# Optimization experiments

Hardware: AMD Instinct MI355X
Metric: run time of the kernel (lower is better)

Reference implementation:

```python
import jax, jax.numpy as jnp
import numpy as np

B, SD, SE, DM, H, DK, DV, DFF = 4, 2048, 2048, 1024, 8, 128, 128, 4096
NEG = -jnp.inf


def _linear(x, w, b):
    # torch nn.Linear: w [out, in]
    return jnp.einsum('...i,oi->...o', x, w) + b


def _layer_norm(x, g, b, eps=1e-5):
    mu = jnp.mean(x, axis=-1, keepdims=True)
    var = jnp.var(x, axis=-1, keepdims=True)
    return (x - mu) * jax.lax.rsqrt(var + eps) * g + b


def _mha(Q, K, V, wq, bq, wk, bk, wv, bv, wo, bo, pad_mask, seq_mask):
    # wq/wk: [H, DK, DM], wv: [H, DV, DM]; vectorized over the per-head Linears
    Qh = jnp.einsum('bsd,hkd->bhsk', Q, wq) + bq[None, :, None, :]  # [B,H,Sq,DK]
    Kh = jnp.einsum('bsd,hkd->bhsk', K, wk) + bk[None, :, None, :]  # [B,H,Sk,DK]
    Vh = jnp.einsum('bsd,hvd->bhsv', V, wv) + bv[None, :, None, :]  # [B,H,Sk,DV]
    scores = jnp.einsum('bhqd,bhkd->bhqk', Qh, Kh) / np.sqrt(DK)
    scores = jnp.where(pad_mask[:, None, :, :] == 0, NEG, scores)
    if seq_mask is not None:
        scores = jnp.where(seq_mask[None, None, :, :] == 0, NEG, scores)
    w = jax.nn.softmax(scores, axis=-1)
    out = jnp.einsum('bhqk,bhkv->bhqv', w, Vh)  # [B,H,Sq,DV]
    out = out.transpose(0, 2, 1, 3).reshape(Q.shape[0], Q.shape[1], H * DV)
    return _linear(out, wo, bo)


def setup_inputs() -> dict:
    key = jax.random.key(0)
    ks = iter(jax.random.split(key, 40))
    s = 0.02
    d = {
        'output_embs': jax.random.normal(next(ks), (B, SD, DM), jnp.float32),
        'encoder_output': jax.random.normal(next(ks), (B, SE, DM), jnp.float32),
        'inputs_padding_mask': jnp.ones((B, 1, SE), jnp.int32),
        'outputs_padding_mask': jnp.ones((B, 1, SD), jnp.int32),
    }
    for name in ['q1', 'k1', 'v1', 'q2', 'k2', 'v2']:
        d[name + '_w'] = jax.random.normal(next(ks), (DM, DM), jnp.float32) * s
        d[name + '_b'] = jnp.zeros((DM,), jnp.float32)
    for p in ['sa', 'ed']:
        d[p + '_qw'] = jax.random.normal(next(ks), (H, DK, DM), jnp.float32) * s
        d[p + '_qb'] = jnp.zeros((H, DK), jnp.float32)
        d[p + '_kw'] = jax.random.normal(next(ks), (H, DK, DM), jnp.float32) * s
        d[p + '_kb'] = jnp.zeros((H, DK), jnp.float32)
        d[p + '_vw'] = jax.random.normal(next(ks), (H, DV, DM), jnp.float32) * s
        d[p + '_vb'] = jnp.zeros((H, DV), jnp.float32)
        d[p + '_ow'] = jax.random.normal(next(ks), (DM, H * DV), jnp.float32) * s
        d[p + '_ob'] = jnp.zeros((DM,), jnp.float32)
    d['ff_w1'] = jax.random.normal(next(ks), (DFF, DM), jnp.float32) * s
    d['ff_b1'] = jnp.zeros((DFF,), jnp.float32)
    d['ff_w2'] = jax.random.normal(next(ks), (DM, DFF), jnp.float32) * s
    d['ff_b2'] = jnp.zeros((DM,), jnp.float32)
    d['ln1_g'] = jnp.ones((DM,), jnp.float32)
    d['ln1_b'] = jnp.zeros((DM,), jnp.float32)
    d['ln2_g'] = jnp.ones((DM,), jnp.float32)
    d['ln2_b'] = jnp.zeros((DM,), jnp.float32)
    return d


def reference(output_embs, encoder_output, inputs_padding_mask, outputs_padding_mask,
              q1_w, q1_b, k1_w, k1_b, v1_w, v1_b,
              q2_w, q2_b, k2_w, k2_b, v2_w, v2_b,
              sa_qw, sa_qb, sa_kw, sa_kb, sa_vw, sa_vb, sa_ow, sa_ob,
              ed_qw, ed_qb, ed_kw, ed_kb, ed_vw, ed_vb, ed_ow, ed_ob,
              ff_w1, ff_b1, ff_w2, ff_b2, ln1_g, ln1_b, ln2_g, ln2_b):
    # Dropout (p=0.1 in torch) treated as identity for a deterministic reference.
    seq_len = output_embs.shape[1]
    seq_mask = jnp.tril(jnp.ones((seq_len, seq_len), jnp.float32))
    Q = _linear(output_embs, q1_w, q1_b)
    K = _linear(output_embs, k1_w, k1_b)
    V = _linear(output_embs, v1_w, v1_b)
    x = output_embs + _mha(Q, K, V, sa_qw, sa_qb, sa_kw, sa_kb, sa_vw, sa_vb,
                           sa_ow, sa_ob, outputs_padding_mask, seq_mask)
    x = _layer_norm(x, ln1_g, ln1_b)
    Q2 = _linear(x, q2_w, q2_b)
    K2 = _linear(encoder_output, k2_w, k2_b)
    V2 = _linear(encoder_output, v2_w, v2_b)
    # NOTE: original adds residual from output_embs (not x) -- kept faithful.
    y = output_embs + _mha(Q2, K2, V2, ed_qw, ed_qb, ed_kw, ed_kb, ed_vw, ed_vb,
                           ed_ow, ed_ob, inputs_padding_mask, None)
    y = _layer_norm(y, ln2_g, ln2_b)
    ff = _linear(jax.nn.relu(_linear(y, ff_w1, ff_b1)), ff_w2, ff_b2)
    out = y + ff
    # original reuses layer_norm2 for the final norm (layer_norm3 unused) -- faithful.
    out = _layer_norm(out, ln2_g, ln2_b)
    return out
```

## Files before the change

kernel.cpp:

```cpp
#include <hip/hip_runtime.h>
#include <hip/hip_bf16.h>

typedef __hip_bfloat16 bf16;
typedef short short8 __attribute__((ext_vector_type(8)));
typedef short short4v __attribute__((ext_vector_type(4)));
typedef float floatx4 __attribute__((ext_vector_type(4)));
typedef int intx4 __attribute__((ext_vector_type(4)));
typedef unsigned int uintx4 __attribute__((ext_vector_type(4)));

#define B_ 4
#define SD_ 2048
#define SE_ 2048
#define DM_ 1024
#define H_ 8
#define DFF_ 4096

__device__ __forceinline__ float b2f(bf16 v) { return __bfloat162float(v); }
__device__ __forceinline__ bf16 f2b(float v) { return __float2bfloat16(v); }
__device__ __forceinline__ short f2s(float v) { return __builtin_bit_cast(short, __float2bfloat16(v)); }

__device__ __forceinline__ unsigned cvtpk_bf16(float lo, float hi) {
    unsigned r;
    asm("v_cvt_pk_bf16_f32 %0, %1, %2" : "=v"(r) : "v"(lo), "v"(hi));
    return r;
}
__device__ __forceinline__ void pl32swap(unsigned &x, unsigned &y) {
    asm("v_permlane32_swap_b32 %0, %1" : "+v"(x), "+v"(y));
}
__device__ __forceinline__ void pl16swap(unsigned &x, unsigned &y) {
    asm("v_permlane16_swap_b32 %0, %1" : "+v"(x), "+v"(y));
}

__device__ __forceinline__ void gl_lds16(const short* g, short* l) {
    __builtin_amdgcn_global_load_lds(
        (const __attribute__((address_space(1))) void*)g,
        (__attribute__((address_space(3))) void*)l, 16, 0, 0);
}

__global__ __launch_bounds__(256) void cvt_f32_bf16(
    const float* __restrict__ in, bf16* __restrict__ out, int n)
{
    int i = (blockIdx.x * 256 + threadIdx.x) * 8;
    if (i >= n) return;
    floatx4 a = *(const floatx4*)(in + i);
    floatx4 b = *(const floatx4*)(in + i + 4);
    short8 r;
#pragma unroll
    for (int k = 0; k < 4; ++k) { r[k] = f2s(a[k]); r[k + 4] = f2s(b[k]); }
    *(short8*)(out + i) = r;
}

__global__ __launch_bounds__(256) void cvt_f32_bf16_T(
    const float* __restrict__ in, bf16* __restrict__ out)
{
    __shared__ short tl[32][36];
    const int tid = threadIdx.x;
    const int i = tid >> 3;
    const int j = (tid & 7) * 4;
    const int r0 = blockIdx.x * 32, c0 = blockIdx.y * 32;
    floatx4 v = *(const floatx4*)(in + (size_t)(r0 + i) * 1024 + c0 + j);
#pragma unroll
    for (int p = 0; p < 4; ++p) tl[i][j + p] = f2s(v[p]);
    __syncthreads();
    short4v r;
#pragma unroll
    for (int p = 0; p < 4; ++p) r[p] = tl[j + p][i];
    *(short4v*)(out + (size_t)(c0 + i) * 1024 + r0 + j) = r;
}

__global__ __launch_bounds__(256) void bias_comp(
    const float* __restrict__ w, const float* __restrict__ bin,
    const float* __restrict__ badd, float* __restrict__ out)
{
    __shared__ float red[4];
    const int o = blockIdx.x;
    const int t = threadIdx.x;
    float s = 0.f;
#pragma unroll
    for (int i = t; i < 1024; i += 256) s += w[(size_t)o * 1024 + i] * bin[i];
#pragma unroll
    for (int off = 32; off >= 1; off >>= 1) s += __shfl_xor(s, off);
    if ((t & 63) == 0) red[t >> 6] = s;
    __syncthreads();
    if (t == 0) out[o] = red[0] + red[1] + red[2] + red[3] + badd[o];
}

template <int RELU>
__global__ __launch_bounds__(256) void gemm_bt(
    const bf16* __restrict__ A, const bf16* __restrict__ W,
    const float* __restrict__ bias, bf16* __restrict__ C,
    int M, int N, int K)
{
    __shared__ __align__(16) short As[16 * 512];
    __shared__ __align__(16) short Ws[16 * 512];

    const int tid  = threadIdx.x;
    const int lane = tid & 63;
    const int wave = tid >> 6;
    const int quad = lane >> 4;
    const int l16  = lane & 15;
    const int r7   = l16 & 7;
    const int bm0  = blockIdx.y * 128;
    const int bn0  = blockIdx.x * 128;
    const int wm   = (wave >> 1) * 64;
    const int wn   = (wave & 1) * 64;

    const int scol = (((lane & 7) ^ (lane >> 3)) * 8);
    const short* Ag = (const short*)A + (size_t)(bm0 + wave * 32 + (lane >> 3)) * K + scol;
    const short* Wg = (const short*)W + (size_t)(bn0 + wave * 32 + (lane >> 3)) * K + scol;
    short* Al = As + (wave * 4) * 512;
    short* Wl = Ws + (wave * 4) * 512;

    floatx4 acc[4][4];
#pragma unroll
    for (int i = 0; i < 4; ++i)
#pragma unroll
        for (int j = 0; j < 4; ++j)
            acc[i][j] = (floatx4){0.f, 0.f, 0.f, 0.f};

    for (int k0 = 0; k0 < K; k0 += 64) {
        __syncthreads();
#pragma unroll
        for (int s = 0; s < 4; ++s) {
            gl_lds16(Ag + k0 + (size_t)s * 8 * K, Al + s * 512);
            gl_lds16(Wg + k0 + (size_t)s * 8 * K, Wl + s * 512);
        }
        __syncthreads();
#pragma unroll
        for (int kk = 0; kk < 64; kk += 32) {
            short8 af[4], bg[4];
#pragma unroll
            for (int i = 0; i < 4; ++i) {
                int row = wm + i * 16 + l16;
                af[i] = *(const short8*)&As[(row >> 3) * 512 + r7 * 64 +
                                            (((quad + (kk >> 3)) ^ r7) << 3)];
            }
#pragma unroll
            for (int j = 0; j < 4; ++j) {
                int row = wn + j * 16 + l16;
                bg[j] = *(const short8*)&Ws[(row >> 3) * 512 + r7 * 64 +
                                            (((quad + (kk >> 3)) ^ r7) << 3)];
            }
#pragma unroll
            for (int i = 0; i < 4; ++i)
#pragma unroll
                for (int j = 0; j < 4; ++j)
                    acc[i][j] = __builtin_amdgcn_mfma_f32_16x16x32_bf16(
                        af[i], bg[j], acc[i][j], 0, 0, 0);
        }
    }

#pragma unroll
    for (int j = 0; j < 4; ++j) {
        int col = bn0 + wn + j * 16 + l16;
        float bv = bias ? bias[col] : 0.f;
#pragma unroll
        for (int i = 0; i < 4; ++i) {
            int row0 = bm0 + wm + i * 16 + quad * 4;
#pragma unroll
            for (int r = 0; r < 4; ++r) {
                float v = acc[i][j][r] + bv;
                if (RELU) v = fmaxf(v, 0.f);
                C[(size_t)(row0 + r) * N + col] = f2b(v);
            }
        }
    }
}

template <int RELU>
__global__ __launch_bounds__(512, 2) void gemm256(
    const bf16* __restrict__ A, const bf16* __restrict__ W,
    const float* __restrict__ bias, bf16* __restrict__ C,
    int M, int N, int K)
{
    __shared__ __align__(16) short L[3 * 24576];

    const int tid  = threadIdx.x;
    const int lane = tid & 63;
    const int wave = tid >> 6;
    const int quad = lane >> 4;
    const int l16  = lane & 15;
    const int r7   = l16 & 7;
    const int wm   = wave >> 1;
    const int wn   = wave & 1;

    const int gx  = gridDim.x;
    const int nwg = gx * gridDim.y;
    int wg = blockIdx.y * gx + blockIdx.x;
    if ((nwg & 7) == 0) wg = (wg & 7) * (nwg >> 3) + (wg >> 3);
    const int bn0 = (wg % gx) * 128;
    const int bm0 = (wg / gx) * 256;

    const int scol = (((lane & 7) ^ ((lane >> 3) & 7)) * 8);
    const short* Ag = (const short*)A + (size_t)(bm0 + wave * 32 + (lane >> 3)) * K + scol;
    const short* Wg = (const short*)W + (size_t)(bn0 + wave * 16 + (lane >> 3)) * K + scol;
    const int aw = (wave * 32) * 64;
    const int bw = 16384 + (wave * 16) * 64;

    floatx4 acc[4][4];
#pragma unroll
    for (int i = 0; i < 4; ++i)
#pragma unroll
        for (int j = 0; j < 4; ++j)
            acc[i][j] = (floatx4){0.f, 0.f, 0.f, 0.f};

    const int T = K / 64;

#pragma unroll
    for (int i = 0; i < 4; ++i) gl_lds16(Ag + (size_t)(i * 8) * K, L + aw + i * 8 * 64);
#pragma unroll
    for (int i = 0; i < 2; ++i) gl_lds16(Wg + (size_t)(i * 8) * K, L + bw + i * 8 * 64);
#pragma unroll
    for (int i = 0; i < 4; ++i) gl_lds16(Ag + 64 + (size_t)(i * 8) * K, L + 24576 + aw + i * 8 * 64);
#pragma unroll
    for (int i = 0; i < 2; ++i) gl_lds16(Wg + 64 + (size_t)(i * 8) * K, L + 24576 + bw + i * 8 * 64);
    asm volatile("s_waitcnt vmcnt(6)" ::: "memory");
    __builtin_amdgcn_s_barrier();

    int cur = 0, stg = 2;
    for (int t = 0; t < T; ++t) {
        __builtin_amdgcn_sched_barrier(0);
        const int kt = (t + 2 < T) ? (t + 2) : (T - 1);
        const size_t kg = (size_t)kt * 64;
        const short* Ac = L + cur * 24576;
        const short* Bc = Ac + 16384;
        short* As_s = L + stg * 24576 + aw;
        short* Bs_s = L + stg * 24576 + bw;

        short8 af[2][2], bf[4][2];

#pragma unroll
        for (int mi = 0; mi < 2; ++mi)
#pragma unroll
            for (int ks = 0; ks < 2; ++ks)
                af[mi][ks] = *(const short8*)&Ac[(wm * 64 + mi * 16 + l16) * 64 +
                                                (((ks * 4 + quad) ^ r7) << 3)];
#pragma unroll
        for (int nf = 0; nf < 4; ++nf)
#pragma unroll
            for (int ks = 0; ks < 2; ++ks)
                bf[nf][ks] = *(const short8*)&Bc[(wn * 64 + nf * 16 + l16) * 64 +
                                                (((ks * 4 + quad) ^ r7) << 3)];
        gl_lds16(Ag + kg, As_s);
        gl_lds16(Ag + kg + (size_t)8 * K, As_s + 8 * 64);
        gl_lds16(Wg + kg, Bs_s);
        __builtin_amdgcn_s_barrier();
        asm volatile("s_waitcnt lgkmcnt(0)" ::: "memory");
        __builtin_amdgcn_sched_barrier(0);
        __builtin_amdgcn_s_setprio(1);
#pragma unroll
        for (int ks = 0; ks < 2; ++ks)
#pragma unroll
            for (int mi = 0; mi < 2; ++mi)
#pragma unroll
                for (int nf = 0; nf < 4; ++nf)
                    acc[mi][nf] = __builtin_amdgcn_mfma_f32_16x16x32_bf16(
                        af[mi][ks], bf[nf][ks], acc[mi][nf], 0, 0, 0);
        __builtin_amdgcn_s_setprio(0);
        __builtin_amdgcn_s_barrier();

#pragma unroll
        for (int mi = 0; mi < 2; ++mi)
#pragma unroll
            for (int ks = 0; ks < 2; ++ks)
                af[mi][ks] = *(const short8*)&Ac[(wm * 64 + (2 + mi) * 16 + l16) * 64 +
                                                (((ks * 4 + quad) ^ r7) << 3)];
        gl_lds16(Ag + kg + (size_t)16 * K, As_s + 16 * 64);
        gl_lds16(Ag + kg + (size_t)24 * K, As_s + 24 * 64);
        gl_lds16(Wg + kg + (size_t)8 * K, Bs_s + 8 * 64);
        __builtin_amdgcn_s_barrier();
        asm volatile("s_waitcnt lgkmcnt(0)" ::: "memory");
        __builtin_amdgcn_sched_barrier(0);
        __builtin_amdgcn_s_setprio(1);
#pragma unroll
        for (int ks = 0; ks < 2; ++ks)
#pragma unroll
            for (int mi = 0; mi < 2; ++mi)
#pragma unroll
                for (int nf = 0; nf < 4; ++nf)
                    acc[2 + mi][nf] = __builtin_amdgcn_mfma_f32_16x16x32_bf16(
                        af[mi][ks], bf[nf][ks], acc[2 + mi][nf], 0, 0, 0);
        __builtin_amdgcn_s_setprio(0);
        asm volatile("s_waitcnt vmcnt(6)" ::: "memory");
        __builtin_amdgcn_s_barrier();

        cur = (cur == 2) ? 0 : cur + 1;
        stg = (stg == 2) ? 0 : stg + 1;
    }

#pragma unroll
    for (int nf = 0; nf < 4; ++nf) {
        int col = bn0 + wn * 64 + nf * 16 + l16;
        float bv = bias ? bias[col] : 0.f;
#pragma unroll
        for (int mf = 0; mf < 4; ++mf) {
            int row0 = bm0 + wm * 64 + mf * 16 + quad * 4;
#pragma unroll
            for (int r = 0; r < 4; ++r) {
                float v = acc[mf][nf][r] + bv;
                if (RELU) v = fmaxf(v, 0.f);
                C[(size_t)(row0 + r) * N + col] = f2b(v);
            }
        }
    }
}

__global__ __launch_bounds__(256) void vtrans(
    const bf16* __restrict__ in, int str, bf16* __restrict__ out, int S)
{
    __shared__ short t[32][36];
    const int tid = threadIdx.x;
    const int s0  = blockIdx.x * 32;
    const int d0  = blockIdx.y * 32;
    const int bh  = blockIdx.z;
    const int b = bh >> 3, h = bh & 7;
    const int i = tid >> 3;
    const int j = (tid & 7) * 4;

    *(short4v*)&t[i][j] =
        *(const short4v*)(in + (size_t)(b * S + s0 + i) * str + h * 128 + d0 + j);
    __syncthreads();
    short4v r;
#pragma unroll
    for (int p = 0; p < 4; ++p) r[p] = t[j + p][i];
    *(short4v*)(out + ((size_t)bh * 128 + d0 + i) * S + s0 + j) = r;
}

template <int CAUSAL>
__global__ __launch_bounds__(256) void flash_attn(
    const bf16* __restrict__ Q, int qstr, const bf16* __restrict__ K, int kstr,
    const bf16* __restrict__ Vt, const int* __restrict__ pad,
    bf16* __restrict__ Of, float* __restrict__ Ls, int Sq, int Sk)
{
    __shared__ __align__(16) short Ks[64 * 128];
    __shared__ __align__(16) short Vs[128 * 64];

    const int tid  = threadIdx.x;
    const int lane = tid & 63;
    const int wave = tid >> 6;
    const int quad = lane >> 4;
    const int l16  = lane & 15;
    const int r7   = l16 & 7;
    const int bh   = blockIdx.y;
    const int b    = bh >> 3;
    const int h    = bh & 7;
    const int par  = blockIdx.z;
    int tile = blockIdx.x;
    if (CAUSAL) tile = (tile & 1) ? (gridDim.x - 1 - (tile >> 1)) : (tile >> 1);
    const int q0 = tile * 128;
    const int qw = q0 + wave * 32;

    short8 qf[2][4];
#pragma unroll
    for (int mi = 0; mi < 2; ++mi) {
        const bf16* qb = Q + (size_t)(b * Sq + qw + mi * 16 + l16) * qstr + h * 128;
#pragma unroll
        for (int c = 0; c < 4; ++c)
            qf[mi][c] = *(const short8*)(qb + c * 32 + quad * 8);
    }

    floatx4 o[2][8];
#pragma unroll
    for (int mi = 0; mi < 2; ++mi)
#pragma unroll
        for (int nf = 0; nf < 8; ++nf) o[mi][nf] = (floatx4){0.f, 0.f, 0.f, 0.f};
    float lsum[2] = {0.f, 0.f};

    const float sc = 0.08838834764831845f * 1.4426950408889634f;
    int kEnd = Sk;
    if (CAUSAL && q0 + 128 < Sk) kEnd = q0 + 128;

    const bf16* vb0 = Vt + (size_t)bh * 128 * Sk;

    for (int ci = par; ci * 64 < kEnd; ci += 2) {
        const int kc = ci * 64;
        __syncthreads();
#pragma unroll
        for (int s = 0; s < 4; ++s) {
            int seg = wave * 4 + s;
            int kr = seg * 4 + (lane >> 4);
            int kg = (lane & 15) ^ (kr & 7);
            gl_lds16((const short*)K + (size_t)(b * Sk + kc + kr) * kstr + h * 128 + kg * 8,
                     Ks + seg * 512);
            int vr = seg * 8 + (lane >> 3);
            int vg = (lane & 7) ^ (vr & 7);
            gl_lds16((const short*)vb0 + (size_t)vr * Sk + kc + vg * 8,
                     Vs + seg * 512);
        }
        __syncthreads();

        short8 pfm[2][2];
#pragma unroll
        for (int c = 0; c < 2; ++c) {
            floatx4 sT[2][2];
#pragma unroll
            for (int fp = 0; fp < 2; ++fp) {
                const int f = c * 2 + fp;
                const int krow = f * 16 + l16;
                short8 kf[4];
#pragma unroll
                for (int cc = 0; cc < 4; ++cc)
                    kf[cc] = *(const short8*)&Ks[krow * 128 + (((cc * 4 + quad) ^ r7) << 3)];
#pragma unroll
                for (int mi = 0; mi < 2; ++mi) {
                    floatx4 s = (floatx4){0.f, 0.f, 0.f, 0.f};
#pragma unroll
                    for (int cc = 0; cc < 4; ++cc)
                        s = __builtin_amdgcn_mfma_f32_16x16x32_bf16(
                            kf[cc], qf[mi][cc], s, 0, 0, 0);
                    sT[mi][fp] = s;
                }
            }

            const int* pb = pad + (size_t)b * Sk + kc + c * 32 + quad * 4;
            intx4 pv0 = *(const intx4*)pb;
            intx4 pv1 = *(const intx4*)(pb + 16);

#pragma unroll
            for (int mi = 0; mi < 2; ++mi) {
                const int qv = qw + mi * 16 + l16;
#pragma unroll
                for (int fp = 0; fp < 2; ++fp) {
#pragma unroll
                    for (int r = 0; r < 4; ++r) {
                        int kk = kc + (c * 2 + fp) * 16 + quad * 4 + r;
                        bool ok = ((fp ? pv1[r] : pv0[r]) != 0);
                        if (CAUSAL) ok = ok && (kk <= qv);
                        float p = ok ? __builtin_amdgcn_exp2f(sT[mi][fp][r] * sc) : 0.f;
                        sT[mi][fp][r] = p;
                        lsum[mi] += p;
                    }
                }
                unsigned wA = cvtpk_bf16(sT[mi][0][0], sT[mi][0][1]);
                unsigned wB = cvtpk_bf16(sT[mi][0][2], sT[mi][0][3]);
                unsigned wC = cvtpk_bf16(sT[mi][1][0], sT[mi][1][1]);
                unsigned wD = cvtpk_bf16(sT[mi][1][2], sT[mi][1][3]);
                pl32swap(wA, wC);
                pl16swap(wA, wC);
                pl32swap(wB, wD);
                pl16swap(wB, wD);
                uintx4 t;
                t[0] = wA; t[1] = wB; t[2] = wC; t[3] = wD;
                pfm[mi][c] = __builtin_bit_cast(short8, t);
            }
        }

#pragma unroll
        for (int nf = 0; nf < 8; ++nf) {
            int vrow = nf * 16 + l16;
            short8 vf0 = *(const short8*)&Vs[vrow * 64 + ((quad ^ r7) << 3)];
            short8 vf1 = *(const short8*)&Vs[vrow * 64 + (((4 + quad) ^ r7) << 3)];
#pragma unroll
            for (int mi = 0; mi < 2; ++mi) {
                o[mi][nf] = __builtin_amdgcn_mfma_f32_16x16x32_bf16(
                    pfm[mi][0], vf0, o[mi][nf], 0, 0, 0);
                o[mi][nf] = __builtin_amdgcn_mfma_f32_16x16x32_bf16(
                    pfm[mi][1], vf1, o[mi][nf], 0, 0, 0);
            }
        }
    }

    bf16* op = Of + (size_t)par * B_ * Sq * DM_;
    float* lp = Ls + (size_t)par * B_ * H_ * Sq;
#pragma unroll
    for (int mi = 0; mi < 2; ++mi) {
        float s = lsum[mi];
        s += __shfl_xor(s, 16);
        s += __shfl_xor(s, 32);
        if (lane < 16)
            lp[(size_t)bh * Sq + qw + mi * 16 + l16] = s;
#pragma unroll
        for (int nf = 0; nf < 8; ++nf)
#pragma unroll
            for (int r = 0; r < 4; ++r) {
                int q = qw + mi * 16 + quad * 4 + r;
                op[(size_t)(b * Sq + q) * DM_ + h * 128 + nf * 16 + l16] =
                    f2b(o[mi][nf][r]);
            }
    }
}

__global__ __launch_bounds__(256) void attn_combine(
    const bf16* __restrict__ Of, const float* __restrict__ Ls,
    bf16* __restrict__ out)
{
    const int row = blockIdx.x;
    const int t = threadIdx.x;
    const int col = t * 4;
    const int h = col >> 7;
    const int b = row >> 11;
    const int q = row & (SD_ - 1);
    const size_t NV = (size_t)B_ * SD_ * DM_;
    const int idx = (b * H_ + h) * SD_ + q;
    float l = Ls[idx] + Ls[B_ * H_ * SD_ + idx];
    float inv = l > 0.f ? 1.f / l : 0.f;
    size_t base = (size_t)row * DM_ + col;
    short4v a0 = *(const short4v*)(Of + base);
    short4v a1 = *(const short4v*)(Of + NV + base);
    short4v r;
#pragma unroll
    for (int i = 0; i < 4; ++i)
        r[i] = f2s((b2f(__builtin_bit_cast(bf16, (short)a0[i])) +
                    b2f(__builtin_bit_cast(bf16, (short)a1[i]))) * inv);
    *(short4v*)(out + base) = r;
}

template <int A32, int O32>
__global__ __launch_bounds__(256) void add_ln(
    const void* __restrict__ Ap, const bf16* __restrict__ Bv,
    const float* __restrict__ g, const float* __restrict__ be,
    void* __restrict__ outp)
{
    const int D = DM_;
    __shared__ float red[8];
    const size_t row = blockIdx.x;
    const int t = threadIdx.x;

    float x[4];
    {
        float av[4];
        if (A32) {
            floatx4 a4 = *(const floatx4*)((const float*)Ap + row * D + t * 4);
#pragma unroll
            for (int i = 0; i < 4; ++i) av[i] = a4[i];
        } else {
            short4v a4 = *(const short4v*)((const bf16*)Ap + row * D + t * 4);
#pragma unroll
            for (int i = 0; i < 4; ++i)
                av[i] = b2f(__builtin_bit_cast(bf16, (short)a4[i]));
        }
        short4v b4 = *(const short4v*)(Bv + row * D + t * 4);
#pragma unroll
        for (int i = 0; i < 4; ++i)
            x[i] = av[i] + b2f(__builtin_bit_cast(bf16, (short)b4[i]));
    }
    float s = 0.f, s2 = 0.f;
#pragma unroll
    for (int i = 0; i < 4; ++i) { s += x[i]; s2 += x[i] * x[i]; }
#pragma unroll
    for (int off = 32; off >= 1; off >>= 1) {
        s  += __shfl_xor(s, off);
        s2 += __shfl_xor(s2, off);
    }
    const int wave = t >> 6;
    if ((t & 63) == 0) { red[wave] = s; red[4 + wave] = s2; }
    __syncthreads();
    s  = red[0] + red[1] + red[2] + red[3];
    s2 = red[4] + red[5] + red[6] + red[7];
    const float mu   = s * (1.f / D);
    const float var  = s2 * (1.f / D) - mu * mu;
    const float rstd = rsqrtf(var + 1e-5f);
#pragma unroll
    for (int i = 0; i < 4; ++i) {
        int idx = t * 4 + i;
        float v = (x[i] - mu) * rstd * g[idx] + be[idx];
        if (O32) ((float*)outp)[row * D + idx] = v;
        else     ((bf16*)outp)[row * D + idx] = f2b(v);
    }
}

extern "C" void kernel_launch(void* const* d_in, const int* in_sizes, int n_in,
                              void* d_out, int out_size, void* d_ws, size_t ws_size,
                              hipStream_t stream)
{
    const float* emb    = (const float*)d_in[0];
    const float* enc    = (const float*)d_in[1];
    const int*  in_pad  = (const int*)d_in[2];
    const int*  out_pad = (const int*)d_in[3];
    const float* q1_w = (const float*)d_in[4];  const float* q1_b = (const float*)d_in[5];
    const float* k1_w = (const float*)d_in[6];  const float* k1_b = (const float*)d_in[7];
    const float* v1_w = (const float*)d_in[8];  const float* v1_b = (const float*)d_in[9];
    const float* q2_w = (const float*)d_in[10]; const float* q2_b = (const float*)d_in[11];
    const float* k2_w = (const float*)d_in[12]; const float* k2_b = (const float*)d_in[13];
    const float* v2_w = (const float*)d_in[14]; const float* v2_b = (const float*)d_in[15];
    const float* sa_qw = (const float*)d_in[16]; const float* sa_qb = (const float*)d_in[17];
    const float* sa_kw = (const float*)d_in[18]; const float* sa_kb = (const float*)d_in[19];
    const float* sa_vw = (const float*)d_in[20]; const float* sa_vb = (const float*)d_in[21];
    const float* sa_ow = (const float*)d_in[22]; const float* sa_ob = (const float*)d_in[23];
    const float* ed_qw = (const float*)d_in[24]; const float* ed_qb = (const float*)d_in[25];
    const float* ed_kw = (const float*)d_in[26]; const float* ed_kb = (const float*)d_in[27];
    const float* ed_vw = (const float*)d_in[28]; const float* ed_vb = (const float*)d_in[29];
    const float* ed_ow = (const float*)d_in[30]; const float* ed_ob = (const float*)d_in[31];
    const float* ff_w1 = (const float*)d_in[32]; const float* ff_b1 = (const float*)d_in[33];
    const float* ff_w2 = (const float*)d_in[34]; const float* ff_b2 = (const float*)d_in[35];
    const float* ln1_g = (const float*)d_in[36]; const float* ln1_b = (const float*)d_in[37];
    const float* ln2_g = (const float*)d_in[38]; const float* ln2_b = (const float*)d_in[39];

    const int M = B_ * SD_;
    const size_t MM = (size_t)1024 * 1024;
    bf16* ws = (bf16*)d_ws;

    bf16* Wqkv = ws;
    bf16* Wkv  = ws + 3 * MM;
    bf16* Wq2  = ws + 5 * MM;
    bf16* Wso  = ws + 6 * MM;
    bf16* Weo  = ws + 7 * MM;
    bf16* Wf1  = ws + 8 * MM;
    bf16* Wf2  = ws + 12 * MM;
    float* bQKV = (float*)(ws + 16 * MM);
    float* bKV  = bQKV + 3072;
    float* bQ2  = bKV + 2048;
    float* Lsum = bQ2 + 2048;
    bf16* hw   = ws + 17 * MM;
    bf16* ft   = ws + 23 * MM;
    bf16* emb_b = ws + 17 * MM;
    bf16* enc_b = ws + 25 * MM;
    bf16* sqkv  = ws + 33 * MM;
    bf16* skv   = ws + 33 * MM;
    bf16* sq2   = ws + 49 * MM;
    bf16* sVt   = ws + 57 * MM;
    bf16* attn  = ws + 65 * MM;
    bf16* Ofb   = ws + 73 * MM;
    bf16* s1    = ws + 73 * MM;
    bf16* x     = ws + 89 * MM;
    bf16* y     = ws + 33 * MM;
    bf16* mid   = ws + 41 * MM;
    bf16* f2    = ws + 81 * MM;

    auto G = [&](const bf16* Ai, const bf16* Wi, const float* bi, bf16* Ci,
                 int Mi, int Ni, int Ki, bool relu) {
        dim3 grid(Ni / 128, Mi / 256);
        if (relu) gemm256<1><<<grid, 512, 0, stream>>>(Ai, Wi, bi, Ci, Mi, Ni, Ki);
        else      gemm256<0><<<grid, 512, 0, stream>>>(Ai, Wi, bi, Ci, Mi, Ni, Ki);
    };
    auto Gp = [&](const bf16* Ai, const bf16* Wi, bf16* Ci) {
        dim3 grid(8, 8);
        gemm_bt<0><<<grid, 256, 0, stream>>>(Ai, Wi, nullptr, Ci, 1024, 1024, 1024);
    };

    const float* hsrc[6] = {sa_qw, sa_kw, sa_vw, ed_qw, ed_kw, ed_vw};
    for (int i = 0; i < 6; ++i)
        cvt_f32_bf16<<<dim3(MM / 2048), 256, 0, stream>>>(hsrc[i], hw + i * MM, (int)MM);
    const float* tsrc[6] = {q1_w, k1_w, v1_w, q2_w, k2_w, v2_w};
    for (int i = 0; i < 6; ++i)
        cvt_f32_bf16_T<<<dim3(32, 32), 256, 0, stream>>>(tsrc[i], ft + i * MM);
    bias_comp<<<dim3(1024), 256, 0, stream>>>(sa_qw, q1_b, sa_qb, bQKV);
    bias_comp<<<dim3(1024), 256, 0, stream>>>(sa_kw, k1_b, sa_kb, bQKV + 1024);
    bias_comp<<<dim3(1024), 256, 0, stream>>>(sa_vw, v1_b, sa_vb, bQKV + 2048);
    bias_comp<<<dim3(1024), 256, 0, stream>>>(ed_kw, k2_b, ed_kb, bKV);
    bias_comp<<<dim3(1024), 256, 0, stream>>>(ed_vw, v2_b, ed_vb, bKV + 1024);
    bias_comp<<<dim3(1024), 256, 0, stream>>>(ed_qw, q2_b, ed_qb, bQ2);
    Gp(hw + 0 * MM, ft + 0 * MM, Wqkv + 0 * MM);
    Gp(hw + 1 * MM, ft + 1 * MM, Wqkv + 1 * MM);
    Gp(hw + 2 * MM, ft + 2 * MM, Wqkv + 2 * MM);
    Gp(hw + 4 * MM, ft + 4 * MM, Wkv  + 0 * MM);
    Gp(hw + 5 * MM, ft + 5 * MM, Wkv  + 1 * MM);
    Gp(hw + 3 * MM, ft + 3 * MM, Wq2);
    cvt_f32_bf16<<<dim3(MM / 2048), 256, 0, stream>>>(sa_ow, Wso, (int)MM);
    cvt_f32_bf16<<<dim3(MM / 2048), 256, 0, stream>>>(ed_ow, Weo, (int)MM);
    cvt_f32_bf16<<<dim3(4 * MM / 2048), 256, 0, stream>>>(ff_w1, Wf1, (int)(4 * MM));
    cvt_f32_bf16<<<dim3(4 * MM / 2048), 256, 0, stream>>>(ff_w2, Wf2, (int)(4 * MM));
    cvt_f32_bf16<<<dim3(8 * MM / 2048), 256, 0, stream>>>(emb, emb_b, (int)(8 * MM));
    cvt_f32_bf16<<<dim3(8 * MM / 2048), 256, 0, stream>>>(enc, enc_b, (int)(8 * MM));

    G(emb_b, Wqkv, bQKV, sqkv, M, 3072, DM_, false);
    vtrans<<<dim3(SD_ / 32, 4, B_ * H_), 256, 0, stream>>>(sqkv + 2048, 3072, sVt, SD_);
    flash_attn<1><<<dim3(SD_ / 128, B_ * H_, 2), 256, 0, stream>>>(
        sqkv, 3072, sqkv + 1024, 3072, sVt, out_pad, Ofb, Lsum, SD_, SD_);
    attn_combine<<<dim3(M), 256, 0, stream>>>(Ofb, Lsum, attn);
    G(attn, Wso, sa_ob, s1, M, DM_, DM_, false);
    add_ln<1, 0><<<dim3(M), 256, 0, stream>>>(emb, s1, ln1_g, ln1_b, x);

    G(enc_b, Wkv, bKV, skv, M, 2048, DM_, false);
    G(x, Wq2, bQ2, sq2, M, DM_, DM_, false);
    vtrans<<<dim3(SE_ / 32, 4, B_ * H_), 256, 0, stream>>>(skv + 1024, 2048, sVt, SE_);
    flash_attn<0><<<dim3(SD_ / 128, B_ * H_, 2), 256, 0, stream>>>(
        sq2, 1024, skv, 2048, sVt, in_pad, Ofb, Lsum, SD_, SE_);
    attn_combine<<<dim3(M), 256, 0, stream>>>(Ofb, Lsum, attn);
    G(attn, Weo, ed_ob, s1, M, DM_, DM_, false);
    add_ln<1, 0><<<dim3(M), 256, 0, stream>>>(emb, s1, ln2_g, ln2_b, y);

    G(y, Wf1, ff_b1, mid, M, DFF_, DM_, true);
    G(mid, Wf2, ff_b2, f2, M, DM_, DFF_, false);
    add_ln<0, 1><<<dim3(M), 256, 0, stream>>>(y, f2, ln2_g, ln2_b, d_out);
}
```

Baseline: 1.028 ms.

## Register-prefetch K/V tiles in flash attention and pair causal tiles per block

The flash attention kernel now loads the next K/V chunk from global memory into registers while the current chunk is computed, then writes it to LDS. This replaces the previous direct global-to-LDS loads that stalled between barriers. For the causal launch, each block processes two query tiles (i and NT-1-i) in sequence, so every block does a balanced amount of work and the grid is halved. It also raises wave priority around the PV MFMA loop. In exchange, register pressure rises from the prefetch buffers, and the smaller causal grid may reduce occupancy.

```diff
diff --git a/kernel.cpp b/kernel.cpp
--- a/kernel.cpp
+++ b/kernel.cpp
@@ -345,138 +345,169 @@
     const int b    = bh >> 3;
     const int h    = bh & 7;
     const int par  = blockIdx.z;
-    int tile = blockIdx.x;
-    if (CAUSAL) tile = (tile & 1) ? (gridDim.x - 1 - (tile >> 1)) : (tile >> 1);
-    const int q0 = tile * 128;
-    const int qw = q0 + wave * 32;
-
-    short8 qf[2][4];
-#pragma unroll
-    for (int mi = 0; mi < 2; ++mi) {
-        const bf16* qb = Q + (size_t)(b * Sq + qw + mi * 16 + l16) * qstr + h * 128;
-#pragma unroll
-        for (int c = 0; c < 4; ++c)
-            qf[mi][c] = *(const short8*)(qb + c * 32 + quad * 8);
-    }
-
-    floatx4 o[2][8];
-#pragma unroll
-    for (int mi = 0; mi < 2; ++mi)
-#pragma unroll
-        for (int nf = 0; nf < 8; ++nf) o[mi][nf] = (floatx4){0.f, 0.f, 0.f, 0.f};
-    float lsum[2] = {0.f, 0.f};
-
+
+    const int NT = Sq >> 7;
     const float sc = 0.08838834764831845f * 1.4426950408889634f;
-    int kEnd = Sk;
-    if (CAUSAL && q0 + 128 < Sk) kEnd = q0 + 128;
-
     const bf16* vb0 = Vt + (size_t)bh * 128 * Sk;
-
-    for (int ci = par; ci * 64 < kEnd; ci += 2) {
-        const int kc = ci * 64;
-        __syncthreads();
-#pragma unroll
-        for (int s = 0; s < 4; ++s) {
-            int seg = wave * 4 + s;
-            int kr = seg * 4 + (lane >> 4);
-            int kg = (lane & 15) ^ (kr & 7);
-            gl_lds16((const short*)K + (size_t)(b * Sk + kc + kr) * kstr + h * 128 + kg * 8,
-                     Ks + seg * 512);
-            int vr = seg * 8 + (lane >> 3);
-            int vg = (lane & 7) ^ (vr & 7);
-            gl_lds16((const short*)vb0 + (size_t)vr * Sk + kc + vg * 8,
-                     Vs + seg * 512);
-        }
-        __syncthreads();
-
-        short8 pfm[2][2];
-#pragma unroll
-        for (int c = 0; c < 2; ++c) {
-            floatx4 sT[2][2];
-#pragma unroll
-            for (int fp = 0; fp < 2; ++fp) {
-                const int f = c * 2 + fp;
-                const int krow = f * 16 + l16;
-                short8 kf[4];
-#pragma unroll
-                for (int cc = 0; cc < 4; ++cc)
-                    kf[cc] = *(const short8*)&Ks[krow * 128 + (((cc * 4 + quad) ^ r7) << 3)];
-#pragma unroll
-                for (int mi = 0; mi < 2; ++mi) {
-                    floatx4 s = (floatx4){0.f, 0.f, 0.f, 0.f};
+    const short* Kb = (const short*)K + (size_t)b * Sk * kstr + h * 128;
+
+    int krr[4], kgg[4], vrr[4], vgg[4];
+#pragma unroll
+    for (int s = 0; s < 4; ++s) {
+        int seg = wave * 4 + s;
+        krr[s] = seg * 4 + (lane >> 4);
+        kgg[s] = (l16 ^ (krr[s] & 7)) * 8;
+        vrr[s] = seg * 8 + (lane >> 3);
+        vgg[s] = ((lane & 7) ^ (vrr[s] & 7)) * 8;
+    }
+
+    const int npass = CAUSAL ? 2 : 1;
+    for (int ps = 0; ps < npass; ++ps) {
+        const int tile = CAUSAL ? (ps ? NT - 1 - (int)blockIdx.x : (int)blockIdx.x)
+                                : (int)blockIdx.x;
+        const int q0 = tile * 128;
+        const int qw = q0 + wave * 32;
+
+        short8 qf[2][4];
+#pragma unroll
+        for (int mi = 0; mi < 2; ++mi) {
+            const bf16* qb = Q + (size_t)(b * Sq + qw + mi * 16 + l16) * qstr + h * 128;
+#pragma unroll
+            for (int c = 0; c < 4; ++c)
+                qf[mi][c] = *(const short8*)(qb + c * 32 + quad * 8);
+        }
+
+        floatx4 o[2][8];
+#pragma unroll
+        for (int mi = 0; mi < 2; ++mi)
+#pragma unroll
+            for (int nf = 0; nf < 8; ++nf) o[mi][nf] = (floatx4){0.f, 0.f, 0.f, 0.f};
+        float lsum[2] = {0.f, 0.f};
+
+        int kEnd = Sk;
+        if (CAUSAL && q0 + 128 < Sk) kEnd = q0 + 128;
+
+        intx4 sk[4], sv[4];
+        {
+            const int kc = par * 64;
+#pragma unroll
+            for (int s = 0; s < 4; ++s) {
+                sk[s] = *(const intx4*)(Kb + (size_t)(kc + krr[s]) * kstr + kgg[s]);
+                sv[s] = *(const intx4*)((const short*)vb0 + (size_t)vrr[s] * Sk + kc + vgg[s]);
+            }
+        }
+
+        for (int ci = par; ci * 64 < kEnd; ci += 2) {
+            const int kc = ci * 64;
+            __syncthreads();
+#pragma unroll
+            for (int s = 0; s < 4; ++s) {
+                *(intx4*)&Ks[(wave * 4 + s) * 512 + lane * 8] = sk[s];
+                *(intx4*)&Vs[(wave * 4 + s) * 512 + lane * 8] = sv[s];
+            }
+            __syncthreads();
+
+            const int kcn = kc + 128;
+            if (kcn < kEnd) {
+#pragma unroll
+                for (int s = 0; s < 4; ++s) {
+                    sk[s] = *(const intx4*)(Kb + (size_t)(kcn + krr[s]) * kstr + kgg[s]);
+                    sv[s] = *(const intx4*)((const short*)vb0 + (size_t)vrr[s] * Sk + kcn + vgg[s]);
+                }
+            }
+            __builtin_amdgcn_sched_barrier(0);
+
+            short8 pfm[2][2];
+#pragma unroll
+            for (int c = 0; c < 2; ++c) {
+                floatx4 sT[2][2];
+#pragma unroll
+                for (int fp = 0; fp < 2; ++fp) {
+                    const int f = c * 2 + fp;
+                    const int krow = f * 16 + l16;
+                    short8 kf[4];
 #pragma unroll
                     for (int cc = 0; cc < 4; ++cc)
-                        s = __builtin_amdgcn_mfma_f32_16x16x32_bf16(
-                            kf[cc], qf[mi][cc], s, 0, 0, 0);
-                    sT[mi][fp] = s;
-                }
-            }
-
-            const int* pb = pad + (size_t)b * Sk + kc + c * 32 + quad * 4;
-            intx4 pv0 = *(const intx4*)pb;
-            intx4 pv1 = *(const intx4*)(pb + 16);
-
-#pragma unroll
-            for (int mi = 0; mi < 2; ++mi) {
-                const int qv = qw + mi * 16 + l16;
-#pragma unroll
-                for (int fp = 0; fp < 2; ++fp) {
-#pragma unroll
-                    for (int r = 0; r < 4; ++r) {
-                        int kk = kc + (c * 2 + fp) * 16 + quad * 4 + r;
-                        bool ok = ((fp ? pv1[r] : pv0[r]) != 0);
-                        if (CAUSAL) ok = ok && (kk <= qv);
-                        float p = ok ? __builtin_amdgcn_exp2f(sT[mi][fp][r] * sc) : 0.f;
-                        sT[mi][fp][r] = p;
-                        lsum[mi] += p;
+                        kf[cc] = *(const short8*)&Ks[krow * 128 + (((cc * 4 + quad) ^ r7) << 3)];
+#pragma unroll
+                    for (int mi = 0; mi < 2; ++mi) {
+                        floatx4 s = (floatx4){0.f, 0.f, 0.f, 0.f};
+#pragma unroll
+                        for (int cc = 0; cc < 4; ++cc)
+                            s = __builtin_amdgcn_mfma_f32_16x16x32_bf16(
+                                kf[cc], qf[mi][cc], s, 0, 0, 0);
+                        sT[mi][fp] = s;
                     }
                 }
-                unsigned wA = cvtpk_bf16(sT[mi][0][0], sT[mi][0][1]);
-                unsigned wB = cvtpk_bf16(sT[mi][0][2], sT[mi][0][3]);
-                unsigned wC = cvtpk_bf16(sT[mi][1][0], sT[mi][1][1]);
-                unsigned wD = cvtpk_bf16(sT[mi][1][2], sT[mi][1][3]);
-                pl32swap(wA, wC);
-                pl16swap(wA, wC);
-                pl32swap(wB, wD);
-                pl16swap(wB, wD);
-                uintx4 t;
-                t[0] = wA; t[1] = wB; t[2] = wC; t[3] = wD;
-                pfm[mi][c] = __builtin_bit_cast(short8, t);
-            }
-        }
-
-#pragma unroll
-        for (int nf = 0; nf < 8; ++nf) {
-            int vrow = nf * 16 + l16;
-            short8 vf0 = *(const short8*)&Vs[vrow * 64 + ((quad ^ r7) << 3)];
-            short8 vf1 = *(const short8*)&Vs[vrow * 64 + (((4 + quad) ^ r7) << 3)];
-#pragma unroll
-            for (int mi = 0; mi < 2; ++mi) {
-                o[mi][nf] = __builtin_amdgcn_mfma_f32_16x16x32_bf16(
-                    pfm[mi][0], vf0, o[mi][nf], 0, 0, 0);
-                o[mi][nf] = __builtin_amdgcn_mfma_f32_16x16x32_bf16(
-                    pfm[mi][1], vf1, o[mi][nf], 0, 0, 0);
-            }
-        }
-    }
-
-    bf16* op = Of + (size_t)par * B_ * Sq * DM_;
-    float* lp = Ls + (size_t)par * B_ * H_ * Sq;
-#pragma unroll
-    for (int mi = 0; mi < 2; ++mi) {
-        float s = lsum[mi];
-        s += __shfl_xor(s, 16);
-        s += __shfl_xor(s, 32);
-        if (lane < 16)
-            lp[(size_t)bh * Sq + qw + mi * 16 + l16] = s;
-#pragma unroll
-        for (int nf = 0; nf < 8; ++nf)
-#pragma unroll
-            for (int r = 0; r < 4; ++r) {
-                int q = qw + mi * 16 + quad * 4 + r;
-                op[(size_t)(b * Sq + q) * DM_ + h * 128 + nf * 16 + l16] =
-                    f2b(o[mi][nf][r]);
-            }
+
+                const int* pb = pad + (size_t)b * Sk + kc + c * 32 + quad * 4;
+                intx4 pv0 = *(const intx4*)pb;
+                intx4 pv1 = *(const intx4*)(pb + 16);
+
+#pragma unroll
+                for (int mi = 0; mi < 2; ++mi) {
+                    const int qv = qw + mi * 16 + l16;
+#pragma unroll
+                    for (int fp = 0; fp < 2; ++fp) {
+#pragma unroll
+                        for (int r = 0; r < 4; ++r) {
+                            int kk = kc + (c * 2 + fp) * 16 + quad * 4 + r;
+                            bool ok = ((fp ? pv1[r] : pv0[r]) != 0);
+                            if (CAUSAL) ok = ok && (kk <= qv);
+                            float p = ok ? __builtin_amdgcn_exp2f(sT[mi][fp][r] * sc) : 0.f;
+                            sT[mi][fp][r] = p;
+                            lsum[mi] += p;
+                        }
+                    }
+                    unsigned wA = cvtpk_bf16(sT[mi][0][0], sT[mi][0][1]);
+                    unsigned wB = cvtpk_bf16(sT[mi][0][2], sT[mi][0][3]);
+                    unsigned wC = cvtpk_bf16(sT[mi][1][0], sT[mi][1][1]);
+                    unsigned wD = cvtpk_bf16(sT[mi][1][2], sT[mi][1][3]);
+                    pl32swap(wA, wC);
+                    pl16swap(wA, wC);
+                    pl32swap(wB, wD);
+                    pl16swap(wB, wD);
+                    uintx4 t;
+                    t[0] = wA; t[1] = wB; t[2] = wC; t[3] = wD;
+                    pfm[mi][c] = __builtin_bit_cast(short8, t);
+                }
+            }
+
+            __builtin_amdgcn_s_setprio(1);
+#pragma unroll
+            for (int nf = 0; nf < 8; ++nf) {
+                int vrow = nf * 16 + l16;
+                short8 vf0 = *(const short8*)&Vs[vrow * 64 + ((quad ^ r7) << 3)];
+                short8 vf1 = *(const short8*)&Vs[vrow * 64 + (((4 + quad) ^ r7) << 3)];
+#pragma unroll
+                for (int mi = 0; mi < 2; ++mi) {
+                    o[mi][nf] = __builtin_amdgcn_mfma_f32_16x16x32_bf16(
+                        pfm[mi][0], vf0, o[mi][nf], 0, 0, 0);
+                    o[mi][nf] = __builtin_amdgcn_mfma_f32_16x16x32_bf16(
+                        pfm[mi][1], vf1, o[mi][nf], 0, 0, 0);
+                }
+            }
+            __builtin_amdgcn_s_setprio(0);
+        }
+
+        bf16* op = Of + (size_t)par * B_ * Sq * DM_;
+        float* lp = Ls + (size_t)par * B_ * H_ * Sq;
+#pragma unroll
+        for (int mi = 0; mi < 2; ++mi) {
+            float s = lsum[mi];
+            s += __shfl_xor(s, 16);
+            s += __shfl_xor(s, 32);
+            if (lane < 16)
+                lp[(size_t)bh * Sq + qw + mi * 16 + l16] = s;
+#pragma unroll
+            for (int nf = 0; nf < 8; ++nf)
+#pragma unroll
+                for (int r = 0; r < 4; ++r) {
+                    int q = qw + mi * 16 + quad * 4 + r;
+                    op[(size_t)(b * Sq + q) * DM_ + h * 128 + nf * 16 + l16] =
+                        f2b(o[mi][nf][r]);
+                }
+        }
     }
 }
 
@@ -655,7 +686,7 @@
 
     G(emb_b, Wqkv, bQKV, sqkv, M, 3072, DM_, false);
     vtrans<<<dim3(SD_ / 32, 4, B_ * H_), 256, 0, stream>>>(sqkv + 2048, 3072, sVt, SD_);
-    flash_attn<1><<<dim3(SD_ / 128, B_ * H_, 2), 256, 0, stream>>>(
+    flash_attn<1><<<dim3(SD_ / 256, B_ * H_, 2), 256, 0, stream>>>(
         sqkv, 3072, sqkv + 1024, 3072, sVt, out_pad, Ofb, Lsum, SD_, SD_);
     attn_combine<<<dim3(M), 256, 0, stream>>>(Ofb, Lsum, attn);
     G(attn, Wso, sa_ob, s1, M, DM_, DM_, false);
```

Result: faster. 1.001 ms (-2.7%).
